# Optimization experiments

Hardware: AMD Instinct MI355X
Metric: run time of the kernel (lower is better)

Reference implementation:

```python
import jax, jax.numpy as jnp
import numpy as np

DIM = 512
HEADS = 8
DIM_HEAD = 64
INNER = HEADS * DIM_HEAD
SCALE = DIM_HEAD ** -0.5


def setup_inputs() -> dict:
    key = jax.random.key(0)
    ks = jax.random.split(key, 6)
    x = jax.random.normal(ks[0], (8, 1024, DIM), dtype=jnp.float32)
    # nn.Linear(dim, inner, bias=False): y = x @ W.T ; store W as [out, in]
    wq = jax.random.normal(ks[1], (INNER, DIM), dtype=jnp.float32) * (DIM ** -0.5)
    wk = jax.random.normal(ks[2], (INNER, DIM), dtype=jnp.float32) * (DIM ** -0.5)
    wv = jax.random.normal(ks[3], (INNER, DIM), dtype=jnp.float32) * (DIM ** -0.5)
    wo = jax.random.normal(ks[4], (DIM, INNER), dtype=jnp.float32) * (INNER ** -0.5)
    bo = jax.random.normal(ks[5], (DIM,), dtype=jnp.float32) * 0.01
    return {"x": x, "wq": wq, "wk": wk, "wv": wv, "wo": wo, "bo": bo}


def reference(x, wq, wk, wv, wo, bo):
    b, n, _ = x.shape
    # QKV projections -> [b, h, n, d]
    def proj(w):
        return (x @ w.T).reshape(b, n, HEADS, DIM_HEAD).transpose(0, 2, 1, 3)
    q, k, v = proj(wq), proj(wk), proj(wv)
    dots = jnp.einsum('bhid,bhjd->bhij', q, k) * SCALE
    dots = jnp.clip(dots, 1e-6, 1.0)
    dots_exp = jnp.exp(dots)
    attn = dots_exp / jnp.sum(dots_exp, axis=-1, keepdims=True)
    out = jnp.einsum('bhij,bhjd->bhid', attn, v)  # [b,h,n,d]
    out = out.transpose(0, 2, 1, 3).reshape(b, n, INNER)
    return out @ wo.T + bo
```

## Files before the change

kernel.cpp:

```cpp
#include <hip/hip_runtime.h>
#include <hip/hip_fp16.h>

#define BATCH 8
#define SEQ   1024
#define DIM   512
#define HEADS 8
#define DHEAD 64
#define MTOT  (BATCH*SEQ)

typedef _Float16 f16x8 __attribute__((ext_vector_type(8)));
typedef _Float16 f16x4 __attribute__((ext_vector_type(4)));
typedef float    fx4   __attribute__((ext_vector_type(4)));

#define MFMA16 __builtin_amdgcn_mfma_f32_16x16x32_f16

__global__ __launch_bounds__(256) void convert_k(
    const float* __restrict__ x,  const float* __restrict__ wq,
    const float* __restrict__ wk, const float* __restrict__ wv,
    const float* __restrict__ wo,
    _Float16* __restrict__ xb, _Float16* __restrict__ wqkvb,
    _Float16* __restrict__ wob)
{
    const int XU = (MTOT*DIM)/4;
    const int WU = (DIM*DIM)/4;
    int idx = blockIdx.x*256 + threadIdx.x;
    if (idx >= XU + 4*WU) return;
    const float* src; _Float16* dst;
    if (idx < XU) { src = x + idx*4; dst = xb + idx*4; }
    else {
        int t = idx - XU; int region = t >> 16; int off = (t & 65535)*4;
        if      (region == 0) { src = wq + off; dst = wqkvb + off; }
        else if (region == 1) { src = wk + off; dst = wqkvb + DIM*DIM + off; }
        else if (region == 2) { src = wv + off; dst = wqkvb + 2*DIM*DIM + off; }
        else                  { src = wo + off; dst = wob + off; }
    }
    float4 v = *(const float4*)src;
    f16x4 o = { (_Float16)v.x, (_Float16)v.y, (_Float16)v.z, (_Float16)v.w };
    *(f16x4*)dst = o;
}

__global__ __launch_bounds__(256,2) void qkv_proj(
    const _Float16* __restrict__ A, const _Float16* __restrict__ B,
    _Float16* __restrict__ Qb, _Float16* __restrict__ Kb,
    _Float16* __restrict__ VTb)
{
    __shared__ _Float16 lA[128*72];
    __shared__ _Float16 lB[128*72];
    const int tid = threadIdx.x;
    const int m0 = blockIdx.y*128, n0 = blockIdx.x*128;
    const int w = tid>>6, l = tid&63, lr = l&15, lq = l>>4;
    const int wr = w>>1, wc = w&1;
    fx4 acc[4][4] = {};

    for (int k0 = 0; k0 < DIM; k0 += 64) {
        __syncthreads();
#pragma unroll
        for (int i = 0; i < 4; i++) {
            int u = tid + i*256;
            int row = u >> 3, cu = (u & 7)*8;
            *(f16x8*)&lA[row*72 + cu] = *(const f16x8*)&A[(m0+row)*DIM + k0 + cu];
            *(f16x8*)&lB[row*72 + cu] = *(const f16x8*)&B[(n0+row)*DIM + k0 + cu];
        }
        __syncthreads();
#pragma unroll
        for (int kb = 0; kb < 2; kb++) {
            f16x8 af[4], bf[4];
#pragma unroll
            for (int cb = 0; cb < 4; cb++)
                bf[cb] = *(const f16x8*)&lB[(wc*64+cb*16+lr)*72 + kb*32 + lq*8];
#pragma unroll
            for (int rb = 0; rb < 4; rb++)
                af[rb] = *(const f16x8*)&lA[(wr*64+rb*16+lr)*72 + kb*32 + lq*8];
#pragma unroll
            for (int rb = 0; rb < 4; rb++)
#pragma unroll
                for (int cb = 0; cb < 4; cb++)
                    acc[rb][cb] = MFMA16(af[rb], bf[cb], acc[rb][cb], 0,0,0);
        }
    }
#pragma unroll
    for (int rb = 0; rb < 4; rb++)
#pragma unroll
        for (int cb = 0; cb < 4; cb++) {
            int nn = n0 + wc*64 + cb*16 + lr;
            int which = nn >> 9, inner = nn & 511, h = inner >> 6, d = inner & 63;
#pragma unroll
            for (int i = 0; i < 4; i++) {
                int m = m0 + wr*64 + rb*16 + lq*4 + i;
                int b = m >> 10, n = m & 1023;
                float v = acc[rb][cb][i];
                if (which == 0)
                    Qb[((b*HEADS+h)*SEQ + n)*DHEAD + d] = (_Float16)(v * 0.125f);
                else if (which == 1)
                    Kb[((b*HEADS+h)*SEQ + n)*DHEAD + d] = (_Float16)v;
                else
                    VTb[((b*HEADS+h)*DHEAD + d)*SEQ + n] = (_Float16)v;
            }
        }
}

__global__ __launch_bounds__(256,2) void attn_k(
    const _Float16* __restrict__ Q, const _Float16* __restrict__ K,
    const _Float16* __restrict__ VT, _Float16* __restrict__ AO)
{
    __shared__ _Float16 lKV[128*72];
    __shared__ _Float16 lP[4][32*136];
    const int tid = threadIdx.x;
    const int w = tid>>6, l = tid&63, lr = l&15, lq = l>>4;
    const int bh = blockIdx.y, q0 = blockIdx.x*128;
    const int b = bh>>3, h = bh&7;
    const _Float16* Qp = Q  + (size_t)bh*SEQ*DHEAD;
    const _Float16* Kp = K  + (size_t)bh*SEQ*DHEAD;
    const _Float16* Vp = VT + (size_t)bh*DHEAD*SEQ;

    f16x8 qf[2][2];
#pragma unroll
    for (int r = 0; r < 2; r++)
#pragma unroll
        for (int kb = 0; kb < 2; kb++)
            qf[r][kb] = *(const f16x8*)&Qp[(q0 + w*32 + r*16 + lr)*DHEAD + kb*32 + lq*8];

    fx4 O[2][4] = {};
    fx4 lsum[2] = {};

    for (int kt = 0; kt < 8; kt++) {
        int k0 = kt*128;
        __syncthreads();
#pragma unroll
        for (int i = 0; i < 4; i++) {
            int u = tid + i*256;
            int row = u >> 3, cu = (u & 7)*8;
            *(f16x8*)&lKV[row*72 + cu] = *(const f16x8*)&Kp[(k0+row)*DHEAD + cu];
        }
        __syncthreads();
#pragma unroll
        for (int cb = 0; cb < 8; cb++) {
            f16x8 kf[2];
#pragma unroll
            for (int kb = 0; kb < 2; kb++)
                kf[kb] = *(const f16x8*)&lKV[(cb*16+lr)*72 + kb*32 + lq*8];
#pragma unroll
            for (int r = 0; r < 2; r++) {
                fx4 s = {};
                s = MFMA16(qf[r][0], kf[0], s, 0,0,0);
                s = MFMA16(qf[r][1], kf[1], s, 0,0,0);
#pragma unroll
                for (int i = 0; i < 4; i++) {
                    float p = __expf(fminf(fmaxf(s[i], 1e-6f), 1.0f));
                    lsum[r][i] += p;
                    lP[w][(r*16 + lq*4 + i)*136 + cb*16 + lr] = (_Float16)p;
                }
            }
        }
        __syncthreads();
#pragma unroll
        for (int i = 0; i < 4; i++) {
            int u = tid + i*256;
            int row = u >> 4, cu = (u & 15)*8;
            *(f16x8*)&lKV[row*136 + cu] = *(const f16x8*)&Vp[row*SEQ + k0 + cu];
        }
        __syncthreads();
#pragma unroll
        for (int ks = 0; ks < 4; ks++) {
            f16x8 af[2];
#pragma unroll
            for (int r = 0; r < 2; r++)
                af[r] = *(const f16x8*)&lP[w][(r*16+lr)*136 + ks*32 + lq*8];
#pragma unroll
            for (int db = 0; db < 4; db++) {
                f16x8 vf = *(const f16x8*)&lKV[(db*16+lr)*136 + ks*32 + lq*8];
                O[0][db] = MFMA16(af[0], vf, O[0][db], 0,0,0);
                O[1][db] = MFMA16(af[1], vf, O[1][db], 0,0,0);
            }
        }
    }
#pragma unroll
    for (int r = 0; r < 2; r++)
#pragma unroll
        for (int i = 0; i < 4; i++) {
            float s = lsum[r][i];
            s += __shfl_xor(s, 1);
            s += __shfl_xor(s, 2);
            s += __shfl_xor(s, 4);
            s += __shfl_xor(s, 8);
            lsum[r][i] = s;
        }
#pragma unroll
    for (int r = 0; r < 2; r++) {
        fx4 inv;
#pragma unroll
        for (int i = 0; i < 4; i++) inv[i] = 1.0f / lsum[r][i];
#pragma unroll
        for (int db = 0; db < 4; db++)
#pragma unroll
            for (int i = 0; i < 4; i++) {
                int n = q0 + w*32 + r*16 + lq*4 + i;
                int d = db*16 + lr;
                AO[((size_t)(b*SEQ + n)*HEADS + h)*DHEAD + d] =
                    (_Float16)(O[r][db][i] * inv[i]);
            }
    }
}

__global__ __launch_bounds__(256,2) void out_proj(
    const _Float16* __restrict__ A, const _Float16* __restrict__ B,
    const float* __restrict__ bo, float* __restrict__ out)
{
    __shared__ _Float16 lA[128*72];
    __shared__ _Float16 lB[128*72];
    const int tid = threadIdx.x;
    const int m0 = blockIdx.y*128, n0 = blockIdx.x*128;
    const int w = tid>>6, l = tid&63, lr = l&15, lq = l>>4;
    const int wr = w>>1, wc = w&1;
    fx4 acc[4][4] = {};

    for (int k0 = 0; k0 < DIM; k0 += 64) {
        __syncthreads();
#pragma unroll
        for (int i = 0; i < 4; i++) {
            int u = tid + i*256;
            int row = u >> 3, cu = (u & 7)*8;
            *(f16x8*)&lA[row*72 + cu] = *(const f16x8*)&A[(m0+row)*DIM + k0 + cu];
            *(f16x8*)&lB[row*72 + cu] = *(const f16x8*)&B[(n0+row)*DIM + k0 + cu];
        }
        __syncthreads();
#pragma unroll
        for (int kb = 0; kb < 2; kb++) {
            f16x8 af[4], bf[4];
#pragma unroll
            for (int cb = 0; cb < 4; cb++)
                bf[cb] = *(const f16x8*)&lB[(wc*64+cb*16+lr)*72 + kb*32 + lq*8];
#pragma unroll
            for (int rb = 0; rb < 4; rb++)
                af[rb] = *(const f16x8*)&lA[(wr*64+rb*16+lr)*72 + kb*32 + lq*8];
#pragma unroll
            for (int rb = 0; rb < 4; rb++)
#pragma unroll
                for (int cb = 0; cb < 4; cb++)
                    acc[rb][cb] = MFMA16(af[rb], bf[cb], acc[rb][cb], 0,0,0);
        }
    }
#pragma unroll
    for (int rb = 0; rb < 4; rb++)
#pragma unroll
        for (int cb = 0; cb < 4; cb++) {
            int nn = n0 + wc*64 + cb*16 + lr;
            float bias = bo[nn];
#pragma unroll
            for (int i = 0; i < 4; i++) {
                int m = m0 + wr*64 + rb*16 + lq*4 + i;
                out[(size_t)m*DIM + nn] = acc[rb][cb][i] + bias;
            }
        }
}

extern "C" void kernel_launch(void* const* d_in, const int* in_sizes, int n_in,
                              void* d_out, int out_size, void* d_ws, size_t ws_size,
                              hipStream_t stream)
{
    const float* x  = (const float*)d_in[0];
    const float* wq = (const float*)d_in[1];
    const float* wk = (const float*)d_in[2];
    const float* wv = (const float*)d_in[3];
    const float* wo = (const float*)d_in[4];
    const float* bo = (const float*)d_in[5];
    float* out = (float*)d_out;
    char* ws = (char*)d_ws;

    _Float16* xb    = (_Float16*)(ws);
    _Float16* wqkvb = (_Float16*)(ws + 8388608);
    _Float16* wob   = (_Float16*)(ws + 9961472);
    _Float16* Qb    = (_Float16*)(ws + 10485760);
    _Float16* Kb    = (_Float16*)(ws + 18874368);
    _Float16* VTb   = (_Float16*)(ws + 27262976);
    _Float16* attnb = (_Float16*)(ws);

    convert_k<<<5120, 256, 0, stream>>>(x, wq, wk, wv, wo, xb, wqkvb, wob);
    qkv_proj<<<dim3(12, 64), 256, 0, stream>>>(xb, wqkvb, Qb, Kb, VTb);
    attn_k<<<dim3(8, 64), 256, 0, stream>>>(Qb, Kb, VTb, attnb);
    out_proj<<<dim3(4, 64), 256, 0, stream>>>(attnb, wob, bo, out);
}
```

Measured before the change: 185.2 us.

## Rework attention to 8 waves of 16 rows, swizzle P, vectorize VT stores

The attention kernel now runs 512 threads per block, with each wave owning 16 query rows instead of 32. This cuts per-wave register use and raises occupancy while the shared K/V tile is loaded cooperatively by more threads. The P buffer in LDS uses an XOR swizzle to reduce bank conflicts, and the clamp uses the fmed3 builtin. The QKV projection kernel splits its epilogue so V-transpose tiles write 4-wide vectorized f16 stores instead of scalar strided stores. The trade-off is fewer MFMAs per K/V fragment load, so K/V reuse per LDS read is lower.

New measurement: 168.9 us. 1.1x faster.

```diff
diff --git a/kernel.cpp b/kernel.cpp
--- a/kernel.cpp
+++ b/kernel.cpp
@@ -78,33 +78,47 @@
                     acc[rb][cb] = MFMA16(af[rb], bf[cb], acc[rb][cb], 0,0,0);
         }
     }
-#pragma unroll
-    for (int rb = 0; rb < 4; rb++)
-#pragma unroll
-        for (int cb = 0; cb < 4; cb++) {
-            int nn = n0 + wc*64 + cb*16 + lr;
-            int which = nn >> 9, inner = nn & 511, h = inner >> 6, d = inner & 63;
-#pragma unroll
-            for (int i = 0; i < 4; i++) {
-                int m = m0 + wr*64 + rb*16 + lq*4 + i;
+    if (n0 >= 1024) {
+#pragma unroll
+        for (int rb = 0; rb < 4; rb++)
+#pragma unroll
+            for (int cb = 0; cb < 4; cb++) {
+                int inner = (n0 - 1024) + wc*64 + cb*16 + lr;
+                int h = inner >> 6, d = inner & 63;
+                int m = m0 + wr*64 + rb*16 + lq*4;
                 int b = m >> 10, n = m & 1023;
-                float v = acc[rb][cb][i];
-                if (which == 0)
-                    Qb[((b*HEADS+h)*SEQ + n)*DHEAD + d] = (_Float16)(v * 0.125f);
-                else if (which == 1)
-                    Kb[((b*HEADS+h)*SEQ + n)*DHEAD + d] = (_Float16)v;
-                else
-                    VTb[((b*HEADS+h)*DHEAD + d)*SEQ + n] = (_Float16)v;
-            }
-        }
-}
-
-__global__ __launch_bounds__(256,2) void attn_k(
+                f16x4 v4;
+#pragma unroll
+                for (int i = 0; i < 4; i++) v4[i] = (_Float16)acc[rb][cb][i];
+                *(f16x4*)&VTb[((size_t)(b*HEADS+h)*DHEAD + d)*SEQ + n] = v4;
+            }
+    } else {
+#pragma unroll
+        for (int rb = 0; rb < 4; rb++)
+#pragma unroll
+            for (int cb = 0; cb < 4; cb++) {
+                int nn = n0 + wc*64 + cb*16 + lr;
+                int which = nn >> 9, inner = nn & 511, h = inner >> 6, d = inner & 63;
+#pragma unroll
+                for (int i = 0; i < 4; i++) {
+                    int m = m0 + wr*64 + rb*16 + lq*4 + i;
+                    int b = m >> 10, n = m & 1023;
+                    float v = acc[rb][cb][i];
+                    if (which == 0)
+                        Qb[((b*HEADS+h)*SEQ + n)*DHEAD + d] = (_Float16)(v * 0.125f);
+                    else
+                        Kb[((b*HEADS+h)*SEQ + n)*DHEAD + d] = (_Float16)v;
+                }
+            }
+    }
+}
+
+__global__ __launch_bounds__(512,4) void attn_k(
     const _Float16* __restrict__ Q, const _Float16* __restrict__ K,
     const _Float16* __restrict__ VT, _Float16* __restrict__ AO)
 {
     __shared__ _Float16 lKV[128*72];
-    __shared__ _Float16 lP[4][32*136];
+    __shared__ _Float16 lP[8][16*136];
     const int tid = threadIdx.x;
     const int w = tid>>6, l = tid&63, lr = l&15, lq = l>>4;
     const int bh = blockIdx.y, q0 = blockIdx.x*128;
@@ -113,22 +127,20 @@
     const _Float16* Kp = K  + (size_t)bh*SEQ*DHEAD;
     const _Float16* Vp = VT + (size_t)bh*DHEAD*SEQ;
 
-    f16x8 qf[2][2];
-#pragma unroll
-    for (int r = 0; r < 2; r++)
-#pragma unroll
-        for (int kb = 0; kb < 2; kb++)
-            qf[r][kb] = *(const f16x8*)&Qp[(q0 + w*32 + r*16 + lr)*DHEAD + kb*32 + lq*8];
-
-    fx4 O[2][4] = {};
-    fx4 lsum[2] = {};
+    f16x8 qf[2];
+#pragma unroll
+    for (int kb = 0; kb < 2; kb++)
+        qf[kb] = *(const f16x8*)&Qp[(q0 + w*16 + lr)*DHEAD + kb*32 + lq*8];
+
+    fx4 O[4] = {};
+    fx4 lsum = {};
 
     for (int kt = 0; kt < 8; kt++) {
         int k0 = kt*128;
         __syncthreads();
 #pragma unroll
-        for (int i = 0; i < 4; i++) {
-            int u = tid + i*256;
+        for (int i = 0; i < 2; i++) {
+            int u = tid + i*512;
             int row = u >> 3, cu = (u & 7)*8;
             *(f16x8*)&lKV[row*72 + cu] = *(const f16x8*)&Kp[(k0+row)*DHEAD + cu];
         }
@@ -139,67 +151,57 @@
 #pragma unroll
             for (int kb = 0; kb < 2; kb++)
                 kf[kb] = *(const f16x8*)&lKV[(cb*16+lr)*72 + kb*32 + lq*8];
-#pragma unroll
-            for (int r = 0; r < 2; r++) {
-                fx4 s = {};
-                s = MFMA16(qf[r][0], kf[0], s, 0,0,0);
-                s = MFMA16(qf[r][1], kf[1], s, 0,0,0);
-#pragma unroll
-                for (int i = 0; i < 4; i++) {
-                    float p = __expf(fminf(fmaxf(s[i], 1e-6f), 1.0f));
-                    lsum[r][i] += p;
-                    lP[w][(r*16 + lq*4 + i)*136 + cb*16 + lr] = (_Float16)p;
-                }
-            }
-        }
-        __syncthreads();
-#pragma unroll
-        for (int i = 0; i < 4; i++) {
-            int u = tid + i*256;
+            fx4 s = {};
+            s = MFMA16(qf[0], kf[0], s, 0,0,0);
+            s = MFMA16(qf[1], kf[1], s, 0,0,0);
+            int pbase = (lq*4)*136 + (((cb*2 + (lr>>3)) ^ (lq<<1))*8) + (lr&7);
+#pragma unroll
+            for (int i = 0; i < 4; i++) {
+                float p = __expf(__builtin_amdgcn_fmed3f(s[i], 1e-6f, 1.0f));
+                lsum[i] += p;
+                lP[w][pbase + i*136] = (_Float16)p;
+            }
+        }
+        __syncthreads();
+#pragma unroll
+        for (int i = 0; i < 2; i++) {
+            int u = tid + i*512;
             int row = u >> 4, cu = (u & 15)*8;
             *(f16x8*)&lKV[row*136 + cu] = *(const f16x8*)&Vp[row*SEQ + k0 + cu];
         }
         __syncthreads();
 #pragma unroll
         for (int ks = 0; ks < 4; ks++) {
-            f16x8 af[2];
-#pragma unroll
-            for (int r = 0; r < 2; r++)
-                af[r] = *(const f16x8*)&lP[w][(r*16+lr)*136 + ks*32 + lq*8];
+            f16x8 af = *(const f16x8*)
+                &lP[w][lr*136 + (((ks*4 + lq) ^ (((lr>>2)&3)<<1))*8)];
 #pragma unroll
             for (int db = 0; db < 4; db++) {
                 f16x8 vf = *(const f16x8*)&lKV[(db*16+lr)*136 + ks*32 + lq*8];
-                O[0][db] = MFMA16(af[0], vf, O[0][db], 0,0,0);
-                O[1][db] = MFMA16(af[1], vf, O[1][db], 0,0,0);
-            }
-        }
-    }
-#pragma unroll
-    for (int r = 0; r < 2; r++)
+                O[db] = MFMA16(af, vf, O[db], 0,0,0);
+            }
+        }
+    }
+#pragma unroll
+    for (int i = 0; i < 4; i++) {
+        float s = lsum[i];
+        s += __shfl_xor(s, 1);
+        s += __shfl_xor(s, 2);
+        s += __shfl_xor(s, 4);
+        s += __shfl_xor(s, 8);
+        lsum[i] = s;
+    }
+    fx4 inv;
+#pragma unroll
+    for (int i = 0; i < 4; i++) inv[i] = 1.0f / lsum[i];
+#pragma unroll
+    for (int db = 0; db < 4; db++)
 #pragma unroll
         for (int i = 0; i < 4; i++) {
-            float s = lsum[r][i];
-            s += __shfl_xor(s, 1);
-            s += __shfl_xor(s, 2);
-            s += __shfl_xor(s, 4);
-            s += __shfl_xor(s, 8);
-            lsum[r][i] = s;
-        }
-#pragma unroll
-    for (int r = 0; r < 2; r++) {
-        fx4 inv;
-#pragma unroll
-        for (int i = 0; i < 4; i++) inv[i] = 1.0f / lsum[r][i];
-#pragma unroll
-        for (int db = 0; db < 4; db++)
-#pragma unroll
-            for (int i = 0; i < 4; i++) {
-                int n = q0 + w*32 + r*16 + lq*4 + i;
-                int d = db*16 + lr;
-                AO[((size_t)(b*SEQ + n)*HEADS + h)*DHEAD + d] =
-                    (_Float16)(O[r][db][i] * inv[i]);
-            }
-    }
+            int n = q0 + w*16 + lq*4 + i;
+            int d = db*16 + lr;
+            AO[((size_t)(b*SEQ + n)*HEADS + h)*DHEAD + d] =
+                (_Float16)(O[db][i] * inv[i]);
+        }
 }
 
 __global__ __launch_bounds__(256,2) void out_proj(
@@ -277,6 +279,6 @@
 
     convert_k<<<5120, 256, 0, stream>>>(x, wq, wk, wv, wo, xb, wqkvb, wob);
     qkv_proj<<<dim3(12, 64), 256, 0, stream>>>(xb, wqkvb, Qb, Kb, VTb);
-    attn_k<<<dim3(8, 64), 256, 0, stream>>>(Qb, Kb, VTb, attnb);
+    attn_k<<<dim3(8, 64), 512, 0, stream>>>(Qb, Kb, VTb, attnb);
     out_proj<<<dim3(4, 64), 256, 0, stream>>>(attnb, wob, bo, out);
 }
```
